# Kernel optimization log

Hardware: AMD Instinct MI355X
Metric: run time of the kernel (lower is better)

Reference implementation:

```python
import jax, jax.numpy as jnp
import numpy as np

B, S, D = 4, 2048, 256
H, RANK, DFF = 8, 8, 1024
DK = D // H
EPS = 1e-5


def _linear(x, W, b):
    # torch nn.Linear: y = x @ W.T + b, W shape (out, in)
    return jnp.einsum('bsd,od->bso', x, W) + b


def _layer_norm(x, g, b):
    mu = jnp.mean(x, axis=-1, keepdims=True)
    var = jnp.var(x, axis=-1, keepdims=True)
    return (x - mu) * jax.lax.rsqrt(var + EPS) * g + b


def setup_inputs() -> dict:
    key = jax.random.key(0)
    ks = jax.random.split(key, 20)
    r = RANK * H
    s = lambda fan_in: 1.0 / np.sqrt(fan_in)
    inp = {
        'x': jax.random.normal(ks[0], (B, S, D), jnp.float32),
        'Wq_down': jax.random.uniform(ks[1], (r, D), jnp.float32, -s(D), s(D)),
        'bq_down': jnp.zeros((r,), jnp.float32),
        'Wq_up': jax.random.uniform(ks[2], (D, r), jnp.float32, -s(r), s(r)),
        'bq_up': jnp.zeros((D,), jnp.float32),
        'Wk_down': jax.random.uniform(ks[3], (r, D), jnp.float32, -s(D), s(D)),
        'bk_down': jnp.zeros((r,), jnp.float32),
        'Wk_up': jax.random.uniform(ks[4], (D, r), jnp.float32, -s(r), s(r)),
        'bk_up': jnp.zeros((D,), jnp.float32),
        'Wv': jax.random.uniform(ks[5], (D, D), jnp.float32, -s(D), s(D)),
        'bv': jnp.zeros((D,), jnp.float32),
        'Wo': jax.random.uniform(ks[6], (D, D), jnp.float32, -s(D), s(D)),
        'bo': jnp.zeros((D,), jnp.float32),
        'ln_attn_g': jnp.ones((D,), jnp.float32),
        'ln_attn_b': jnp.zeros((D,), jnp.float32),
        'W_ff1': jax.random.uniform(ks[7], (DFF, D), jnp.float32, -s(D), s(D)),
        'b_ff1': jnp.zeros((DFF,), jnp.float32),
        'W_ff2': jax.random.uniform(ks[8], (D, DFF), jnp.float32, -s(DFF), s(DFF)),
        'b_ff2': jnp.zeros((D,), jnp.float32),
        'ln_blk_g': jnp.ones((D,), jnp.float32),
        'ln_blk_b': jnp.zeros((D,), jnp.float32),
    }
    return inp


def reference(x, Wq_down, bq_down, Wq_up, bq_up, Wk_down, bk_down, Wk_up, bk_up,
              Wv, bv, Wo, bo, ln_attn_g, ln_attn_b,
              W_ff1, b_ff1, W_ff2, b_ff2, ln_blk_g, ln_blk_b):
    # Low-rank Q/K: down-project to rank*H then up-project to D
    Q = _linear(_linear(x, Wq_down, bq_down), Wq_up, bq_up)
    K = _linear(_linear(x, Wk_down, bk_down), Wk_up, bk_up)
    V = _linear(x, Wv, bv)
    # (B,S,D) -> (B,H,S,DK)
    Q = Q.reshape(B, S, H, DK).transpose(0, 2, 1, 3)
    K = K.reshape(B, S, H, DK).transpose(0, 2, 1, 3)
    V = V.reshape(B, S, H, DK).transpose(0, 2, 1, 3)
    scale = 1.0 / np.sqrt(DK).astype(np.float32)
    scores = jnp.einsum('bhqd,bhkd->bhqk', Q, K) * scale
    attn = jax.nn.softmax(scores, axis=-1)
    context = jnp.einsum('bhqk,bhkd->bhqd', attn, V)
    context = context.transpose(0, 2, 1, 3).reshape(B, S, D)
    attn_out = _linear(context, Wo, bo)
    attn_out = _layer_norm(x + attn_out, ln_attn_g, ln_attn_b)
    # FFN: Linear -> GELU (exact erf, torch default) -> Linear
    h = jax.nn.gelu(_linear(attn_out, W_ff1, b_ff1), approximate=False)
    ff = _linear(h, W_ff2, b_ff2)
    return _layer_norm(attn_out + ff, ln_blk_g, ln_blk_b)
```

## Files before the change

### kernel.cpp

```cpp
#include <hip/hip_runtime.h>
#include <hip/hip_bf16.h>
#include <math.h>

#define NB 4
#define NS 2048
#define ND 256
#define NH 8
#define NDK 32
#define NDFF 1024
#define NROWS (NB * NS)
#define KC 4
#define KVB 64
#define KTILES (NS / KC / KVB)
#define QVLD 384

using short8 = __attribute__((ext_vector_type(8))) short;
using f32x4  = __attribute__((ext_vector_type(4))) float;

__device__ __forceinline__ unsigned short f2bf(float f) {
  union { float f; unsigned u; } v; v.f = f;
  unsigned r = v.u + 0x7fffu + ((v.u >> 16) & 1u);
  return (unsigned short)(r >> 16);
}
__device__ __forceinline__ float bf2f(unsigned short u) {
  union { unsigned u; float f; } v; v.u = ((unsigned)u) << 16;
  return v.f;
}
__device__ __forceinline__ unsigned cvt_pk_bf16(float lo, float hi) {
  unsigned r;
  asm("v_cvt_pk_bf16_f32 %0, %1, %2" : "=v"(r) : "v"(lo), "v"(hi));
  return r;
}
__device__ __forceinline__ void gl_lds16(const void* g, void* l) {
  __builtin_amdgcn_global_load_lds(
      (const __attribute__((address_space(1))) unsigned int*)g,
      (__attribute__((address_space(3))) unsigned int*)l, 16, 0, 0);
}

__global__ void cvt_batch(const float* s0, const float* s1, const float* s2,
                          const float* s3, const float* s4, const float* s5,
                          const float* s6, const float* s7,
                          unsigned short* d0, unsigned short* d1,
                          unsigned short* d2, unsigned short* d3,
                          unsigned short* d4, unsigned short* d5,
                          unsigned short* d6, unsigned short* d7,
                          int n0, int n1, int n2, int n3, int n4, int n5,
                          int n6, int n7) {
  const float* s; unsigned short* d; int n;
  switch (blockIdx.y) {
    case 0: s = s0; d = d0; n = n0; break;
    case 1: s = s1; d = d1; n = n1; break;
    case 2: s = s2; d = d2; n = n2; break;
    case 3: s = s3; d = d3; n = n3; break;
    case 4: s = s4; d = d4; n = n4; break;
    case 5: s = s5; d = d5; n = n5; break;
    case 6: s = s6; d = d6; n = n6; break;
    default: s = s7; d = d7; n = n7; break;
  }
  for (int i = (blockIdx.x * 256 + threadIdx.x) * 4; i < n; i += 256 * 256 * 4) {
    float4 v = *reinterpret_cast<const float4*>(s + i);
    ushort4 o;
    o.x = f2bf(v.x); o.y = f2bf(v.y); o.z = f2bf(v.z); o.w = f2bf(v.w);
    *reinterpret_cast<ushort4*>(d + i) = o;
  }
}

template <int BM, int BN, int ACT, int OBF, int RES, int DUAL, int AF32,
          int ACOMB>
__global__ __launch_bounds__(256)
void gemm_nt(const void* __restrict__ Araw, int lda,
             const unsigned short* __restrict__ W,
             const float* __restrict__ bias, const float* __restrict__ bias2,
             int bsplit, const float* __restrict__ bias3, int bsplit2,
             const float* __restrict__ resid, void* __restrict__ outp,
             int K, int O,
             const void* A2, const unsigned short* W2,
             const float* biasB, void* outp2,
             const unsigned short* paccp, const float* plp) {
  constexpr int MFW = BM / 32;
  constexpr int NFW = BN / 32;
  __shared__ __align__(16) unsigned short lA[2][BM * 64];
  __shared__ __align__(16) unsigned short lB[2][BN * 64];
  const int tid = threadIdx.x, lane = tid & 63, wid = tid >> 6;
  const int wr = wid >> 1, wc = wid & 1;
  const int l15 = lane & 15, lg = lane >> 4;
  const int bm = blockIdx.x, bn = blockIdx.y;

  const void* Ap = Araw;
  const unsigned short* Wp = W;
  const float* biasp = bias;
  void* outpp = outp;
  if (DUAL && blockIdx.z) { Ap = A2; Wp = W2; biasp = biasB; outpp = outp2; }

  auto stage = [&](int k0, int buf) {
#pragma unroll
    for (int it = 0; it < BM / 32; ++it) {
      int c = it * 256 + tid;
      int row = c >> 3, cc = (c & 7) ^ (row & 7);
      if (ACOMB) {
        int g = k0 + cc * 8;
        int grow = bm * BM + row;
        int b = grow >> 11, q = grow & 2047;
        int h = g >> 5, d = g & 31;
        size_t base = ((size_t)(b * 8 + h) * 2048 + q) * 32 + d;
        size_t lbase = (size_t)(b * 8 + h) * 2048 + q;
        float o0 = 0, o1 = 0, o2 = 0, o3 = 0, o4 = 0, o5 = 0, o6 = 0, o7 = 0;
        float L = 0.0f;
#pragma unroll
        for (int c2 = 0; c2 < KC; ++c2) {
          short8 a8 = *reinterpret_cast<const short8*>(
              paccp + (size_t)c2 * 2097152 + base);
          o0 += bf2f((unsigned short)a8[0]);
          o1 += bf2f((unsigned short)a8[1]);
          o2 += bf2f((unsigned short)a8[2]);
          o3 += bf2f((unsigned short)a8[3]);
          o4 += bf2f((unsigned short)a8[4]);
          o5 += bf2f((unsigned short)a8[5]);
          o6 += bf2f((unsigned short)a8[6]);
          o7 += bf2f((unsigned short)a8[7]);
          L += plp[(size_t)c2 * 65536 + lbase];
        }
        float inv = 1.0f / L;
        uint4 w;
        w.x = cvt_pk_bf16(o0 * inv, o1 * inv);
        w.y = cvt_pk_bf16(o2 * inv, o3 * inv);
        w.z = cvt_pk_bf16(o4 * inv, o5 * inv);
        w.w = cvt_pk_bf16(o6 * inv, o7 * inv);
        *reinterpret_cast<uint4*>(&lA[buf][c * 8]) = w;
      } else if (AF32) {
        const float* src =
            (const float*)Ap + (size_t)(bm * BM + row) * lda + k0 + cc * 8;
        float4 v0 = *reinterpret_cast<const float4*>(src);
        float4 v1 = *reinterpret_cast<const float4*>(src + 4);
        uint4 w;
        w.x = cvt_pk_bf16(v0.x, v0.y);
        w.y = cvt_pk_bf16(v0.z, v0.w);
        w.z = cvt_pk_bf16(v1.x, v1.y);
        w.w = cvt_pk_bf16(v1.z, v1.w);
        *reinterpret_cast<uint4*>(&lA[buf][c * 8]) = w;
      } else {
        gl_lds16((const unsigned short*)Ap +
                     (size_t)(bm * BM + row) * lda + k0 + cc * 8,
                 &lA[buf][c * 8]);
      }
    }
#pragma unroll
    for (int it = 0; it < BN / 32; ++it) {
      int c = it * 256 + tid;
      int row = c >> 3, cc = (c & 7) ^ (row & 7);
      gl_lds16(Wp + (size_t)(bn * BN + row) * K + k0 + cc * 8, &lB[buf][c * 8]);
    }
  };

  f32x4 acc[MFW][NFW];
#pragma unroll
  for (int i = 0; i < MFW; ++i)
#pragma unroll
    for (int j = 0; j < NFW; ++j) acc[i][j] = (f32x4)0.0f;

  const int T = K >> 6;
  stage(0, 0);
  __syncthreads();
  for (int t = 0; t < T; ++t) {
    const int cur = t & 1;
    if (t + 1 < T) stage((t + 1) << 6, cur ^ 1);
#pragma unroll
    for (int kk = 0; kk < 2; ++kk) {
      short8 a[MFW], b[NFW];
#pragma unroll
      for (int mf = 0; mf < MFW; ++mf) {
        int row = wr * (BM / 2) + mf * 16 + l15;
        a[mf] = *reinterpret_cast<const short8*>(
            &lA[cur][row * 64 + (((kk * 4 + lg) ^ (l15 & 7)) << 3)]);
      }
#pragma unroll
      for (int nf = 0; nf < NFW; ++nf) {
        int row = wc * (BN / 2) + nf * 16 + l15;
        b[nf] = *reinterpret_cast<const short8*>(
            &lB[cur][row * 64 + (((kk * 4 + lg) ^ (l15 & 7)) << 3)]);
      }
#pragma unroll
      for (int mf = 0; mf < MFW; ++mf)
#pragma unroll
        for (int nf = 0; nf < NFW; ++nf)
          acc[mf][nf] = __builtin_amdgcn_mfma_f32_16x16x32_bf16(
              a[mf], b[nf], acc[mf][nf], 0, 0, 0);
    }
    __syncthreads();
  }

#pragma unroll
  for (int mf = 0; mf < MFW; ++mf)
#pragma unroll
    for (int nf = 0; nf < NFW; ++nf) {
      int col = bn * BN + wc * (BN / 2) + nf * 16 + l15;
      float bv;
      if (bias3 && col >= bsplit2) bv = bias3[col - bsplit2];
      else if (bias2 && col >= bsplit) bv = bias2[col - bsplit];
      else bv = biasp[col];
#pragma unroll
      for (int i = 0; i < 4; ++i) {
        int row = bm * BM + wr * (BM / 2) + mf * 16 + lg * 4 + i;
        float v = acc[mf][nf][i] + bv;
        if (ACT == 1) v = 0.5f * v * (1.0f + erff(v * 0.70710678118654752f));
        if (RES) v += resid[(size_t)row * O + col];
        if (OBF)
          ((unsigned short*)outpp)[(size_t)row * O + col] = f2bf(v);
        else
          ((float*)outpp)[(size_t)row * O + col] = v;
      }
    }
}

__global__ __launch_bounds__(256)
void attn_kernel(const unsigned short* __restrict__ Qb,
                 const unsigned short* __restrict__ Kb,
                 const unsigned short* __restrict__ qv,
                 unsigned short* __restrict__ pacc,
                 float* __restrict__ pl) {
  __shared__ __align__(16) unsigned short lK[2][KVB * 32];
  __shared__ __align__(16) unsigned short lVt[2][32 * 72];
  __shared__ __align__(16) unsigned short lP[4][2][16 * 64];
  const int tid = threadIdx.x, lane = tid & 63, wid = tid >> 6;
  const int l15 = lane & 15, lg = lane >> 4;
  const int bh = blockIdx.x, qt = blockIdx.y, kc = blockIdx.z;
  const int b = bh >> 3, h = bh & 7;
  const size_t headoff = (size_t)h * NDK;
  const int qbase = qt * 128 + wid * 32;
  const int kv0 = kc * (NS / KC);
  const float qscale = 0.25508686f;

  short8 aq[2];
#pragma unroll
  for (int r = 0; r < 2; ++r) {
    short8 v = *reinterpret_cast<const short8*>(
        Qb + (size_t)(b * NS + qbase + r * 16 + l15) * ND + headoff + lg * 8);
#pragma unroll
    for (int j = 0; j < 8; ++j)
      v[j] = (short)f2bf(bf2f((unsigned short)v[j]) * qscale);
    aq[r] = v;
  }

  const unsigned short* kptr =
      Kb + (size_t)(b * NS + kv0 + (tid >> 2)) * ND + headoff +
      (((tid & 3) ^ ((tid >> 3) & 3)) << 3);
  const int vd0 = (tid & 15) * 2, vk0 = (tid >> 4) * 4;
  const unsigned short* vptr =
      qv + (size_t)(b * NS + kv0 + vk0) * QVLD + 128 + headoff + vd0;

  auto writeV = [&](const unsigned* w, int buf) {
    unsigned lo0 = (w[0] & 0xffffu) | (w[1] << 16);
    unsigned lo1 = (w[2] & 0xffffu) | (w[3] << 16);
    unsigned hi0 = (w[0] >> 16) | (w[1] & 0xffff0000u);
    unsigned hi1 = (w[2] >> 16) | (w[3] & 0xffff0000u);
    *reinterpret_cast<uint2*>(&lVt[buf][vd0 * 72 + vk0]) = make_uint2(lo0, lo1);
    *reinterpret_cast<uint2*>(&lVt[buf][(vd0 + 1) * 72 + vk0]) =
        make_uint2(hi0, hi1);
  };

  f32x4 accT[2][2];
#pragma unroll
  for (int r = 0; r < 2; ++r)
#pragma unroll
    for (int d = 0; d < 2; ++d) accT[r][d] = (f32x4)0.0f;
  float l[2] = {0.0f, 0.0f};

  unsigned vr[4];
  gl_lds16(kptr, &lK[0][tid * 8]);
#pragma unroll
  for (int u = 0; u < 4; ++u)
    vr[u] = *reinterpret_cast<const unsigned*>(vptr + (size_t)u * QVLD);
  writeV(vr, 0);
  __syncthreads();

  for (int kt = 0; kt < KTILES; ++kt) {
    const int cur = kt & 1, nxt = cur ^ 1;
    const bool pf = (kt + 1 < KTILES);
    if (pf) {
      kptr += (size_t)KVB * ND;
      vptr += (size_t)KVB * QVLD;
      gl_lds16(kptr, &lK[nxt][tid * 8]);
#pragma unroll
      for (int u = 0; u < 4; ++u)
        vr[u] = *reinterpret_cast<const unsigned*>(vptr + (size_t)u * QVLD);
    }

    f32x4 sT[2][4];
    __builtin_amdgcn_s_setprio(1);
#pragma unroll
    for (int r = 0; r < 2; ++r)
#pragma unroll
      for (int t = 0; t < 4; ++t) {
        short8 bk = *reinterpret_cast<const short8*>(
            &lK[cur][(t * 16 + l15) * 32 + ((lg ^ ((l15 >> 1) & 3)) << 3)]);
        sT[r][t] = __builtin_amdgcn_mfma_f32_16x16x32_bf16(
            bk, aq[r], (f32x4)0.0f, 0, 0, 0);
      }
    __builtin_amdgcn_s_setprio(0);

#pragma unroll
    for (int r = 0; r < 2; ++r)
#pragma unroll
      for (int t = 0; t < 4; ++t) {
        float p0 = __builtin_amdgcn_exp2f(sT[r][t][0]);
        float p1 = __builtin_amdgcn_exp2f(sT[r][t][1]);
        float p2 = __builtin_amdgcn_exp2f(sT[r][t][2]);
        float p3 = __builtin_amdgcn_exp2f(sT[r][t][3]);
        l[r] += (p0 + p1) + (p2 + p3);
        unsigned w0 = cvt_pk_bf16(p0, p1);
        unsigned w1 = cvt_pk_bf16(p2, p3);
        int blk = (t << 1) | (lg >> 1);
        *reinterpret_cast<uint2*>(
            &lP[wid][r][l15 * 64 + ((blk ^ (l15 & 7)) << 3) +
                        ((lg & 1) << 2)]) = make_uint2(w0, w1);
      }

    __builtin_amdgcn_s_setprio(1);
#pragma unroll
    for (int r = 0; r < 2; ++r)
#pragma unroll
      for (int kk = 0; kk < 2; ++kk) {
        short8 pa = *reinterpret_cast<const short8*>(
            &lP[wid][r][l15 * 64 + (((kk * 4 + lg) ^ (l15 & 7)) << 3)]);
#pragma unroll
        for (int dt = 0; dt < 2; ++dt) {
          short8 bv = *reinterpret_cast<const short8*>(
              &lVt[cur][(dt * 16 + l15) * 72 + kk * 32 + lg * 8]);
          accT[r][dt] = __builtin_amdgcn_mfma_f32_16x16x32_bf16(
              bv, pa, accT[r][dt], 0, 0, 0);
        }
      }
    __builtin_amdgcn_s_setprio(0);

    if (pf) writeV(vr, nxt);
    __syncthreads();
  }

#pragma unroll
  for (int r = 0; r < 2; ++r) {
    l[r] += __shfl_xor(l[r], 16);
    l[r] += __shfl_xor(l[r], 32);
  }

#pragma unroll
  for (int r = 0; r < 2; ++r) {
    int qg = qbase + r * 16 + l15;
    size_t rowbase = ((size_t)kc * 65536 + (size_t)bh * NS + qg) * 32;
#pragma unroll
    for (int dt = 0; dt < 2; ++dt) {
      unsigned w0 = cvt_pk_bf16(accT[r][dt][0], accT[r][dt][1]);
      unsigned w1 = cvt_pk_bf16(accT[r][dt][2], accT[r][dt][3]);
      *reinterpret_cast<uint2*>(&pacc[rowbase + dt * 16 + lg * 4]) =
          make_uint2(w0, w1);
    }
  }
  if (lane < 16) {
#pragma unroll
    for (int r = 0; r < 2; ++r) {
      int qg = qbase + r * 16 + l15;
      pl[(size_t)kc * 65536 + (size_t)bh * NS + qg] = l[r];
    }
  }
}

__global__ __launch_bounds__(256)
void ln_res_kernel(const float* __restrict__ a,
                   const float* __restrict__ g, const float* __restrict__ be,
                   float* yf, unsigned short* yb) {
  int row = blockIdx.x * 4 + (threadIdx.x >> 6);
  int lane = threadIdx.x & 63;
  size_t off = (size_t)row * ND + lane * 4;
  float4 va = *reinterpret_cast<const float4*>(a + off);
  float v0 = va.x, v1 = va.y, v2 = va.z, v3 = va.w;
  float s = v0 + v1 + v2 + v3;
  float sq = v0 * v0 + v1 * v1 + v2 * v2 + v3 * v3;
#pragma unroll
  for (int o = 1; o < 64; o <<= 1) {
    s += __shfl_xor(s, o);
    sq += __shfl_xor(sq, o);
  }
  float mu = s * (1.0f / 256.0f);
  float var = sq * (1.0f / 256.0f) - mu * mu;
  float rs = rsqrtf(var + 1e-5f);
  float4 vg = *reinterpret_cast<const float4*>(g + lane * 4);
  float4 vbe = *reinterpret_cast<const float4*>(be + lane * 4);
  float o0 = (v0 - mu) * rs * vg.x + vbe.x;
  float o1 = (v1 - mu) * rs * vg.y + vbe.y;
  float o2 = (v2 - mu) * rs * vg.z + vbe.z;
  float o3 = (v3 - mu) * rs * vg.w + vbe.w;
  if (yf) *reinterpret_cast<float4*>(yf + off) = make_float4(o0, o1, o2, o3);
  if (yb) {
    ushort4 ob;
    ob.x = f2bf(o0); ob.y = f2bf(o1); ob.z = f2bf(o2); ob.w = f2bf(o3);
    *reinterpret_cast<ushort4*>(yb + off) = ob;
  }
}

extern "C" void kernel_launch(void* const* d_in, const int* in_sizes, int n_in,
                              void* d_out, int out_size, void* d_ws,
                              size_t ws_size, hipStream_t stream) {
  (void)in_sizes; (void)n_in; (void)out_size; (void)ws_size;
  const float* x   = (const float*)d_in[0];
  const float* Wqd = (const float*)d_in[1];
  const float* bqd = (const float*)d_in[2];
  const float* Wqu = (const float*)d_in[3];
  const float* bqu = (const float*)d_in[4];
  const float* Wkd = (const float*)d_in[5];
  const float* bkd = (const float*)d_in[6];
  const float* Wku = (const float*)d_in[7];
  const float* bku = (const float*)d_in[8];
  const float* Wv  = (const float*)d_in[9];
  const float* bv  = (const float*)d_in[10];
  const float* Wo  = (const float*)d_in[11];
  const float* bo  = (const float*)d_in[12];
  const float* g1  = (const float*)d_in[13];
  const float* be1 = (const float*)d_in[14];
  const float* Wf1 = (const float*)d_in[15];
  const float* bf1 = (const float*)d_in[16];
  const float* Wf2 = (const float*)d_in[17];
  const float* bf2 = (const float*)d_in[18];
  const float* g2  = (const float*)d_in[19];
  const float* be2 = (const float*)d_in[20];

  char* p = (char*)d_ws;
  auto alloc = [&](size_t bytes) {
    char* r = p;
    p += (bytes + 255) & ~(size_t)255;
    return r;
  };
  unsigned short* wqkv = (unsigned short*)alloc(384 * 256 * 2);
  unsigned short* wqu  = (unsigned short*)alloc(256 * 64 * 2);
  unsigned short* wku  = (unsigned short*)alloc(256 * 64 * 2);
  unsigned short* wo   = (unsigned short*)alloc(256 * 256 * 2);
  unsigned short* wf1  = (unsigned short*)alloc(1024 * 256 * 2);
  unsigned short* wf2  = (unsigned short*)alloc(256 * 1024 * 2);
  unsigned short* qv   = (unsigned short*)alloc((size_t)NROWS * QVLD * 2);
  unsigned short* Qb   = (unsigned short*)alloc((size_t)NROWS * ND * 2);
  unsigned short* Kb   = (unsigned short*)alloc((size_t)NROWS * ND * 2);
  float*          y1   = (float*)alloc((size_t)NROWS * ND * 4);
  unsigned short* y1b  = (unsigned short*)alloc((size_t)NROWS * ND * 2);
  unsigned short* hb   = (unsigned short*)alloc((size_t)NROWS * NDFF * 2);
  float* ao = (float*)d_out;

  unsigned short* pacc = hb;
  float* pl = y1;

  cvt_batch<<<dim3(256, 8), 256, 0, stream>>>(
      Wqd, Wkd, Wqu, Wku, Wv, Wo, Wf1, Wf2,
      wqkv, wqkv + 64 * 256, wqu, wku, wqkv + 128 * 256, wo, wf1, wf2,
      64 * 256, 64 * 256, 256 * 64, 256 * 64, 256 * 256,
      256 * 256, 1024 * 256, 256 * 1024);

  gemm_nt<64, 64, 0, 1, 0, 0, 1, 0><<<dim3(128, 6), 256, 0, stream>>>(
      x, 256, wqkv, bqd, bkd, 64, bv, 128, nullptr, qv, 256, QVLD,
      nullptr, nullptr, nullptr, nullptr, nullptr, nullptr);
  gemm_nt<64, 64, 0, 1, 0, 1, 0, 0><<<dim3(128, 4, 2), 256, 0, stream>>>(
      qv, QVLD, wqu, bqu, nullptr, 0, nullptr, 0, nullptr, Qb, 64, 256,
      qv + 64, wku, bku, Kb, nullptr, nullptr);

  attn_kernel<<<dim3(NB * NH, NS / 128, KC), 256, 0, stream>>>(
      Qb, Kb, qv, pacc, pl);

  gemm_nt<64, 64, 0, 0, 1, 0, 0, 1><<<dim3(128, 4), 256, 0, stream>>>(
      nullptr, 256, wo, bo, nullptr, 0, nullptr, 0, x, ao, 256, 256,
      nullptr, nullptr, nullptr, nullptr, pacc, pl);
  ln_res_kernel<<<NROWS / 4, 256, 0, stream>>>(ao, g1, be1, y1, y1b);

  gemm_nt<128, 128, 1, 1, 0, 0, 0, 0><<<dim3(64, 8), 256, 0, stream>>>(
      y1b, 256, wf1, bf1, nullptr, 0, nullptr, 0, nullptr, hb, 256, NDFF,
      nullptr, nullptr, nullptr, nullptr, nullptr, nullptr);
  gemm_nt<64, 64, 0, 0, 1, 0, 0, 0><<<dim3(128, 4), 256, 0, stream>>>(
      hb, 1024, wf2, bf2, nullptr, 0, nullptr, 0, y1, ao, 1024, 256,
      nullptr, nullptr, nullptr, nullptr, nullptr, nullptr);
  ln_res_kernel<<<NROWS / 4, 256, 0, stream>>>(ao, g2, be2,
                                               (float*)d_out, nullptr);
}
```

Measured before the change: 109.2 us.

## Drop fp32 LN1 output, read bf16 residual in FF2, restructure attention LDS

The first layer norm no longer writes an fp32 copy. The FF2 GEMM epilogue now reads the bf16 y1b as its residual through a new RES==2 mode, which saves one fp32 write and one fp32 read of the activation. The attention kernel processes the two query sub-tiles one at a time, so it needs a single P buffer per wave, and V^T is stored with an XOR-swizzled 64-wide layout instead of padding. Together these cut LDS use and register pressure. The cost is a bf16-rounded residual in the second layer norm, which is a small accuracy loss.

```diff
diff --git a/kernel.cpp b/kernel.cpp
--- a/kernel.cpp
+++ b/kernel.cpp
@@ -72,7 +72,7 @@
              const unsigned short* __restrict__ W,
              const float* __restrict__ bias, const float* __restrict__ bias2,
              int bsplit, const float* __restrict__ bias3, int bsplit2,
-             const float* __restrict__ resid, void* __restrict__ outp,
+             const void* __restrict__ resid, void* __restrict__ outp,
              int K, int O,
              const void* A2, const unsigned short* W2,
              const float* biasB, void* outp2,
@@ -203,7 +203,10 @@
         int row = bm * BM + wr * (BM / 2) + mf * 16 + lg * 4 + i;
         float v = acc[mf][nf][i] + bv;
         if (ACT == 1) v = 0.5f * v * (1.0f + erff(v * 0.70710678118654752f));
-        if (RES) v += resid[(size_t)row * O + col];
+        if (RES == 1)
+          v += ((const float*)resid)[(size_t)row * O + col];
+        else if (RES == 2)
+          v += bf2f(((const unsigned short*)resid)[(size_t)row * O + col]);
         if (OBF)
           ((unsigned short*)outpp)[(size_t)row * O + col] = f2bf(v);
         else
@@ -219,8 +222,8 @@
                  unsigned short* __restrict__ pacc,
                  float* __restrict__ pl) {
   __shared__ __align__(16) unsigned short lK[2][KVB * 32];
-  __shared__ __align__(16) unsigned short lVt[2][32 * 72];
-  __shared__ __align__(16) unsigned short lP[4][2][16 * 64];
+  __shared__ __align__(16) unsigned short lVt[2][32 * 64];
+  __shared__ __align__(16) unsigned short lP[4][16 * 64];
   const int tid = threadIdx.x, lane = tid & 63, wid = tid >> 6;
   const int l15 = lane & 15, lg = lane >> 4;
   const int bh = blockIdx.x, qt = blockIdx.y, kc = blockIdx.z;
@@ -244,17 +247,19 @@
   const unsigned short* kptr =
       Kb + (size_t)(b * NS + kv0 + (tid >> 2)) * ND + headoff +
       (((tid & 3) ^ ((tid >> 3) & 3)) << 3);
-  const int vd0 = (tid & 15) * 2, vk0 = (tid >> 4) * 4;
+  const int vd0 = (tid & 15) * 2, vb = tid >> 4;
   const unsigned short* vptr =
-      qv + (size_t)(b * NS + kv0 + vk0) * QVLD + 128 + headoff + vd0;
+      qv + (size_t)(b * NS + kv0 + vb * 4) * QVLD + 128 + headoff + vd0;
+  const int vbs = vb ^ ((((tid & 15) * 2 >> 1) & 7) << 1);
 
   auto writeV = [&](const unsigned* w, int buf) {
     unsigned lo0 = (w[0] & 0xffffu) | (w[1] << 16);
     unsigned lo1 = (w[2] & 0xffffu) | (w[3] << 16);
     unsigned hi0 = (w[0] >> 16) | (w[1] & 0xffff0000u);
     unsigned hi1 = (w[2] >> 16) | (w[3] & 0xffff0000u);
-    *reinterpret_cast<uint2*>(&lVt[buf][vd0 * 72 + vk0]) = make_uint2(lo0, lo1);
-    *reinterpret_cast<uint2*>(&lVt[buf][(vd0 + 1) * 72 + vk0]) =
+    *reinterpret_cast<uint2*>(&lVt[buf][vd0 * 64 + vbs * 4]) =
+        make_uint2(lo0, lo1);
+    *reinterpret_cast<uint2*>(&lVt[buf][(vd0 + 1) * 64 + vbs * 4]) =
         make_uint2(hi0, hi1);
   };
 
@@ -285,52 +290,49 @@
         vr[u] = *reinterpret_cast<const unsigned*>(vptr + (size_t)u * QVLD);
     }
 
-    f32x4 sT[2][4];
-    __builtin_amdgcn_s_setprio(1);
-#pragma unroll
-    for (int r = 0; r < 2; ++r)
+#pragma unroll
+    for (int r = 0; r < 2; ++r) {
+      f32x4 sT[4];
+      __builtin_amdgcn_s_setprio(1);
 #pragma unroll
       for (int t = 0; t < 4; ++t) {
         short8 bk = *reinterpret_cast<const short8*>(
             &lK[cur][(t * 16 + l15) * 32 + ((lg ^ ((l15 >> 1) & 3)) << 3)]);
-        sT[r][t] = __builtin_amdgcn_mfma_f32_16x16x32_bf16(
+        sT[t] = __builtin_amdgcn_mfma_f32_16x16x32_bf16(
             bk, aq[r], (f32x4)0.0f, 0, 0, 0);
       }
-    __builtin_amdgcn_s_setprio(0);
-
-#pragma unroll
-    for (int r = 0; r < 2; ++r)
+      __builtin_amdgcn_s_setprio(0);
 #pragma unroll
       for (int t = 0; t < 4; ++t) {
-        float p0 = __builtin_amdgcn_exp2f(sT[r][t][0]);
-        float p1 = __builtin_amdgcn_exp2f(sT[r][t][1]);
-        float p2 = __builtin_amdgcn_exp2f(sT[r][t][2]);
-        float p3 = __builtin_amdgcn_exp2f(sT[r][t][3]);
+        float p0 = __builtin_amdgcn_exp2f(sT[t][0]);
+        float p1 = __builtin_amdgcn_exp2f(sT[t][1]);
+        float p2 = __builtin_amdgcn_exp2f(sT[t][2]);
+        float p3 = __builtin_amdgcn_exp2f(sT[t][3]);
         l[r] += (p0 + p1) + (p2 + p3);
         unsigned w0 = cvt_pk_bf16(p0, p1);
         unsigned w1 = cvt_pk_bf16(p2, p3);
         int blk = (t << 1) | (lg >> 1);
         *reinterpret_cast<uint2*>(
-            &lP[wid][r][l15 * 64 + ((blk ^ (l15 & 7)) << 3) +
-                        ((lg & 1) << 2)]) = make_uint2(w0, w1);
-      }
-
-    __builtin_amdgcn_s_setprio(1);
-#pragma unroll
-    for (int r = 0; r < 2; ++r)
+            &lP[wid][l15 * 64 + ((blk ^ (l15 & 7)) << 3) + ((lg & 1) << 2)]) =
+            make_uint2(w0, w1);
+      }
+      __builtin_amdgcn_s_setprio(1);
 #pragma unroll
       for (int kk = 0; kk < 2; ++kk) {
         short8 pa = *reinterpret_cast<const short8*>(
-            &lP[wid][r][l15 * 64 + (((kk * 4 + lg) ^ (l15 & 7)) << 3)]);
+            &lP[wid][l15 * 64 + (((kk * 4 + lg) ^ (l15 & 7)) << 3)]);
 #pragma unroll
         for (int dt = 0; dt < 2; ++dt) {
+          int row = dt * 16 + l15;
+          int bb = ((kk * 4 + lg) << 1) ^ (((l15 >> 1) & 7) << 1);
           short8 bv = *reinterpret_cast<const short8*>(
-              &lVt[cur][(dt * 16 + l15) * 72 + kk * 32 + lg * 8]);
+              &lVt[cur][row * 64 + (bb << 2)]);
           accT[r][dt] = __builtin_amdgcn_mfma_f32_16x16x32_bf16(
               bv, pa, accT[r][dt], 0, 0, 0);
         }
       }
-    __builtin_amdgcn_s_setprio(0);
+      __builtin_amdgcn_s_setprio(0);
+    }
 
     if (pf) writeV(vr, nxt);
     __syncthreads();
@@ -437,13 +439,12 @@
   unsigned short* qv   = (unsigned short*)alloc((size_t)NROWS * QVLD * 2);
   unsigned short* Qb   = (unsigned short*)alloc((size_t)NROWS * ND * 2);
   unsigned short* Kb   = (unsigned short*)alloc((size_t)NROWS * ND * 2);
-  float*          y1   = (float*)alloc((size_t)NROWS * ND * 4);
+  float*          pl   = (float*)alloc((size_t)KC * 65536 * 4);
   unsigned short* y1b  = (unsigned short*)alloc((size_t)NROWS * ND * 2);
   unsigned short* hb   = (unsigned short*)alloc((size_t)NROWS * NDFF * 2);
   float* ao = (float*)d_out;
 
   unsigned short* pacc = hb;
-  float* pl = y1;
 
   cvt_batch<<<dim3(256, 8), 256, 0, stream>>>(
       Wqd, Wkd, Wqu, Wku, Wv, Wo, Wf1, Wf2,
@@ -464,13 +465,13 @@
   gemm_nt<64, 64, 0, 0, 1, 0, 0, 1><<<dim3(128, 4), 256, 0, stream>>>(
       nullptr, 256, wo, bo, nullptr, 0, nullptr, 0, x, ao, 256, 256,
       nullptr, nullptr, nullptr, nullptr, pacc, pl);
-  ln_res_kernel<<<NROWS / 4, 256, 0, stream>>>(ao, g1, be1, y1, y1b);
+  ln_res_kernel<<<NROWS / 4, 256, 0, stream>>>(ao, g1, be1, nullptr, y1b);
 
   gemm_nt<128, 128, 1, 1, 0, 0, 0, 0><<<dim3(64, 8), 256, 0, stream>>>(
       y1b, 256, wf1, bf1, nullptr, 0, nullptr, 0, nullptr, hb, 256, NDFF,
       nullptr, nullptr, nullptr, nullptr, nullptr, nullptr);
-  gemm_nt<64, 64, 0, 0, 1, 0, 0, 0><<<dim3(128, 4), 256, 0, stream>>>(
-      hb, 1024, wf2, bf2, nullptr, 0, nullptr, 0, y1, ao, 1024, 256,
+  gemm_nt<64, 64, 0, 0, 2, 0, 0, 0><<<dim3(128, 4), 256, 0, stream>>>(
+      hb, 1024, wf2, bf2, nullptr, 0, nullptr, 0, y1b, ao, 1024, 256,
       nullptr, nullptr, nullptr, nullptr, nullptr, nullptr);
   ln_res_kernel<<<NROWS / 4, 256, 0, stream>>>(ao, g2, be2,
                                                (float*)d_out, nullptr);
```

After: 106.7 us. 1.02x faster.
